# Kernel tuning notes

Hardware: AMD Instinct MI355X
Metric: run time of the kernel (lower is better)

The kernel has to match this reference:

```python
import jax, jax.numpy as jnp
import numpy as np

N_NODES, N_EDGES = 100000, 1000000
D_NODE, D_EDGE, HIDDEN = 64, 32, 64
THRESHOLD = 0.5


def _linear_params(key, out_dim, in_dim):
    # torch.nn.Linear default init: U(-1/sqrt(in), 1/sqrt(in)) for W and b
    kw, kb = jax.random.split(key)
    bound = 1.0 / np.sqrt(in_dim)
    W = jax.random.uniform(kw, (out_dim, in_dim), jnp.float32, -bound, bound)
    b = jax.random.uniform(kb, (out_dim,), jnp.float32, -bound, bound)
    return W, b


def setup_inputs() -> dict:
    key = jax.random.key(0)
    ks = jax.random.split(key, 6)
    node_features = jax.random.normal(ks[0], (N_NODES, D_NODE), jnp.float32)
    edge_index = jax.random.randint(ks[1], (2, N_EDGES), 0, N_NODES, dtype=jnp.int64)
    edge_features = jax.random.normal(ks[2], (N_EDGES, D_EDGE), jnp.float32)
    d_in = 2 * D_NODE + D_EDGE
    W1, b1 = _linear_params(ks[3], HIDDEN, d_in)
    W2, b2 = _linear_params(ks[4], HIDDEN // 2, HIDDEN)
    W3, b3 = _linear_params(ks[5], 1, HIDDEN // 2)
    return {
        "node_features": node_features,
        "edge_index": edge_index,
        "edge_features": edge_features,
        "W1": W1, "b1": b1, "W2": W2, "b2": b2, "W3": W3, "b3": b3,
    }


def reference(node_features, edge_index, edge_features, W1, b1, W2, b2, W3, b3):
    # Gather endpoint features for every edge: [E, D_NODE] each
    src = node_features[edge_index[0]]
    tgt = node_features[edge_index[1]]
    combined = jnp.concatenate([src, tgt, edge_features], axis=1)  # [E, 2*Dn+De]
    x = jax.nn.relu(combined @ W1.T + b1)
    x = jax.nn.relu(x @ W2.T + b2)
    edge_scores = jax.nn.sigmoid((x @ W3.T + b3).squeeze(-1))  # [E]
    keep_mask = edge_scores >= THRESHOLD  # edges with score < threshold removed
    return edge_scores, keep_mask
```

## Files before the change

kernel.cpp:

```cpp
#include <hip/hip_runtime.h>
#include <math.h>

#define N_NODES 100000
#define NE 1000000
#define D_NODE 64
#define D_EDGE 32
#define HID 64
#define H2C 32
#define D_IN 160
#define NTILES (NE / 16)
#define CHUNK 8
#define EPS1 1.5e-3f
#define EPS2 1e-3f

typedef __attribute__((ext_vector_type(8))) short short8;
typedef __attribute__((ext_vector_type(4))) float f32x4;

#define WS_A1_OFF 16
#define WS_A2_OFF (WS_A1_OFF + 8192)
#define WS_AS_OFF (WS_A2_OFF + 8192)
#define WS_AT_OFF (WS_AS_OFF + 16384)
#define WS_UHI    (WS_AT_OFF + 16384)
#define TBL_BYTES (N_NODES * HID * 2)
#define WS_ULO (WS_UHI + TBL_BYTES)
#define WS_VHI (WS_ULO + TBL_BYTES)
#define WS_VLO (WS_VHI + TBL_BYTES)
#define WS_MASK (WS_VLO + TBL_BYTES)
#define WS_MASK2 (WS_MASK + 125008)
#define WS_V15_MIN (WS_MASK2 + 125008 + 131072)

__device__ __forceinline__ unsigned short bf16_rne(float x) {
    unsigned int u = __float_as_uint(x);
    u += 0x7fffu + ((u >> 16) & 1u);
    return (unsigned short)(u >> 16);
}
__device__ __forceinline__ float bf16_tof(unsigned short h) {
    return __uint_as_float(((unsigned int)h) << 16);
}
__device__ __forceinline__ float h2f(unsigned short h) {
    _Float16 x = *reinterpret_cast<const _Float16*>(&h);
    return (float)x;
}
__device__ __forceinline__ unsigned short f2h(float f) {
    _Float16 x = (_Float16)f;
    return *reinterpret_cast<const unsigned short*>(&x);
}
__device__ __forceinline__ void split8(const float* xs, short8& hi, short8& lo) {
    #pragma unroll
    for (int i = 0; i < 8; ++i) {
        unsigned short h = bf16_rne(xs[i]);
        float fh = bf16_tof(h);
        unsigned short l = bf16_rne(xs[i] - fh);
        hi[i] = (short)h;
        lo[i] = (short)l;
    }
}

__global__ void prep_pack_v15(const float* __restrict__ W1, const float* __restrict__ W2,
                              unsigned char* __restrict__ ws)
{
    const int t = blockIdx.x * blockDim.x + threadIdx.x;
    if (t == 0) { *(int*)ws = 0; }
    unsigned short* a1 = (unsigned short*)(ws + WS_A1_OFF);
    unsigned short* a2 = (unsigned short*)(ws + WS_A2_OFF);
    unsigned short* as_ = (unsigned short*)(ws + WS_AS_OFF);
    unsigned short* at_ = (unsigned short*)(ws + WS_AT_OFF);
    for (int task = t; task < 1536; task += gridDim.x * blockDim.x) {
        const int l = task & 63;
        const int l15 = l & 15, kg = l >> 4;
        const float* src;
        unsigned short* dst;
        if (task < 256) {
            const int f = task >> 6;
            src = W1 + (size_t)(f*16 + l15)*D_IN + 128 + kg*8;
            dst = a1 + ((size_t)f*64 + l)*16;
        } else if (task < 512) {
            const int f = (task - 256) >> 6;
            const int nn2 = f >> 1, kk = f & 1;
            src = W2 + (size_t)(nn2*16 + l15)*HID + kk*32 + kg*8;
            dst = a2 + ((size_t)f*64 + l)*16;
        } else if (task < 1024) {
            const int f = (task - 512) >> 6;
            const int nn = f >> 1, kk = f & 1;
            src = W1 + (size_t)(nn*16 + l15)*D_IN + kk*32 + kg*8;
            dst = as_ + ((size_t)f*64 + l)*16;
        } else {
            const int f = (task - 1024) >> 6;
            const int nn = f >> 1, kk = f & 1;
            src = W1 + (size_t)(nn*16 + l15)*D_IN + 64 + kk*32 + kg*8;
            dst = at_ + ((size_t)f*64 + l)*16;
        }
        #pragma unroll
        for (int i = 0; i < 8; ++i) {
            const float wv = src[i];
            const unsigned short h = bf16_rne(wv);
            dst[i] = h;
            dst[8+i] = bf16_rne(wv - bf16_tof(h));
        }
    }
}

__global__ __launch_bounds__(256) void prep_uv_v15(
    const float* __restrict__ nf, const float* __restrict__ b1,
    const unsigned short* __restrict__ asp, const unsigned short* __restrict__ atp,
    unsigned short* __restrict__ Uhi, unsigned short* __restrict__ Ulo,
    unsigned short* __restrict__ Vhi, unsigned short* __restrict__ Vlo)
{
    __shared__ __attribute__((aligned(16))) unsigned short tb[4][16 * 64];
    const int wave = threadIdx.x >> 6, lane = threadIdx.x & 63;
    const int l15 = lane & 15, kg = lane >> 4;
    const int mt = blockIdx.x * 4 + wave;
    if (mt >= N_NODES / 16) return;
    const int node0 = mt * 16;

    const float* np_ = nf + (size_t)(node0 + l15) * 64;
    short8 ahi[2], alo[2];
    #pragma unroll
    for (int kk = 0; kk < 2; ++kk) {
        const float4 x0 = *(const float4*)(np_ + kk*32 + kg*8);
        const float4 x1 = *(const float4*)(np_ + kk*32 + kg*8 + 4);
        float xs[8] = {x0.x,x0.y,x0.z,x0.w,x1.x,x1.y,x1.z,x1.w};
        split8(xs, ahi[kk], alo[kk]);
    }
    float b1v[4];
    #pragma unroll
    for (int nn = 0; nn < 4; ++nn) b1v[nn] = b1[nn*16 + l15];

    const f32x4 z4 = {0.f,0.f,0.f,0.f};
    f32x4 au[4], av[4];
    #pragma unroll
    for (int nn = 0; nn < 4; ++nn) { au[nn] = z4; av[nn] = z4; }
    #pragma unroll
    for (int kk = 0; kk < 2; ++kk) {
        #pragma unroll
        for (int nn = 0; nn < 4; ++nn) {
            const unsigned short* fs = asp + ((size_t)(nn*2+kk)*64 + lane)*16;
            const short8 bsh = *(const short8*)fs;
            const short8 bsl = *(const short8*)(fs + 8);
            au[nn] = __builtin_amdgcn_mfma_f32_16x16x32_bf16(ahi[kk], bsh, au[nn],0,0,0);
            au[nn] = __builtin_amdgcn_mfma_f32_16x16x32_bf16(ahi[kk], bsl, au[nn],0,0,0);
            au[nn] = __builtin_amdgcn_mfma_f32_16x16x32_bf16(alo[kk], bsh, au[nn],0,0,0);
            const unsigned short* ft = atp + ((size_t)(nn*2+kk)*64 + lane)*16;
            const short8 bth = *(const short8*)ft;
            const short8 btl = *(const short8*)(ft + 8);
            av[nn] = __builtin_amdgcn_mfma_f32_16x16x32_bf16(ahi[kk], bth, av[nn],0,0,0);
            av[nn] = __builtin_amdgcn_mfma_f32_16x16x32_bf16(ahi[kk], btl, av[nn],0,0,0);
            av[nn] = __builtin_amdgcn_mfma_f32_16x16x32_bf16(alo[kk], bth, av[nn],0,0,0);
        }
    }

    unsigned short uhr[4][4], ulr[4][4], vhr[4][4], vlr[4][4];
    #pragma unroll
    for (int nn = 0; nn < 4; ++nn)
        #pragma unroll
        for (int r = 0; r < 4; ++r) {
            const float u = au[nn][r] + b1v[nn];
            const unsigned short uh_ = f2h(u);
            uhr[nn][r] = uh_; ulr[nn][r] = f2h(u - h2f(uh_));
            const float v = av[nn][r];
            const unsigned short vh_ = f2h(v);
            vhr[nn][r] = vh_; vlr[nn][r] = f2h(v - h2f(vh_));
        }

    const int tnode = lane >> 2, tsl = lane & 3;
    unsigned short* const dsts[4] = {Uhi, Ulo, Vhi, Vlo};
    #pragma unroll
    for (int pass = 0; pass < 4; ++pass) {
        #pragma unroll
        for (int nn = 0; nn < 4; ++nn)
            #pragma unroll
            for (int r = 0; r < 4; ++r)
                tb[wave][(kg*4 + r)*64 + nn*16 + l15] =
                    (pass == 0) ? uhr[nn][r] :
                    (pass == 1) ? ulr[nn][r] :
                    (pass == 2) ? vhr[nn][r] : vlr[nn][r];
        asm volatile("s_waitcnt lgkmcnt(0)" ::: "memory");
        const uint4 q0 = *(const uint4*)&tb[wave][tnode*64 + tsl*16];
        const uint4 q1 = *(const uint4*)&tb[wave][tnode*64 + tsl*16 + 8];
        unsigned short* gd = dsts[pass] + (size_t)(node0 + tnode)*64 + tsl*16;
        *(uint4*)gd = q0;
        *(uint4*)(gd + 8) = q1;
        asm volatile("s_waitcnt lgkmcnt(0)" ::: "memory");
    }
}

__global__ __launch_bounds__(256) void edge_mlp_v8_kernel(
    const int* __restrict__ ei, const float* __restrict__ ef,
    const float* __restrict__ b2, const float* __restrict__ W3, const float* __restrict__ b3,
    const unsigned short* __restrict__ a1p, const unsigned short* __restrict__ a2p,
    const unsigned short* __restrict__ Uhi, const unsigned short* __restrict__ Vhi,
    unsigned short* __restrict__ maskbuf,
    float* __restrict__ out)
{
    __shared__ __attribute__((aligned(16))) float Hs[4][16][68];
    const int wave = threadIdx.x >> 6, lane = threadIdx.x & 63;
    const int l15 = lane & 15, kg = lane >> 4;
    const long long e0 = (long long)blockIdx.x * 128 + wave * 32;

    const int is64 = (ei[1]==0)&(ei[3]==0)&(ei[5]==0)&(ei[7]==0);

    int si[2], ti[2];
    const float* efpp[2];
    #pragma unroll
    for (int t = 0; t < 2; ++t) {
        long long e = e0 + t * 16 + l15;
        if (e >= NE) e = NE - 1;
        if (is64) { si[t] = ei[(size_t)(2*e)]; ti[t] = ei[(size_t)(2*(NE+e))]; }
        else      { si[t] = ei[(size_t)e];     ti[t] = ei[(size_t)(NE+e)]; }
        efpp[t] = ef + (size_t)e * D_EDGE;
    }
    float4 efv[2][2];
    #pragma unroll
    for (int t = 0; t < 2; ++t) {
        efv[t][0] = *(const float4*)(efpp[t] + kg*8);
        efv[t][1] = *(const float4*)(efpp[t] + kg*8 + 4);
    }
    short8 uh[2][2], vh[2][2];
    #pragma unroll
    for (int t = 0; t < 2; ++t)
        #pragma unroll
        for (int kk = 0; kk < 2; ++kk) {
            uh[t][kk] = *(const short8*)(Uhi + (size_t)si[t]*64 + kk*32 + kg*8);
            vh[t][kk] = *(const short8*)(Vhi + (size_t)ti[t]*64 + kk*32 + kg*8);
        }

    const f32x4 z4 = {0.f,0.f,0.f,0.f};
    f32x4 acc1[2][4];
    #pragma unroll
    for (int t = 0; t < 2; ++t) {
        float xsl[8] = {efv[t][0].x,efv[t][0].y,efv[t][0].z,efv[t][0].w,
                        efv[t][1].x,efv[t][1].y,efv[t][1].z,efv[t][1].w};
        short8 ahi, alo;
        split8(xsl, ahi, alo);
        #pragma unroll
        for (int nn = 0; nn < 4; ++nn) {
            const unsigned short* fp = a1p + ((size_t)nn*64 + lane)*16;
            const short8 bhi = *(const short8*)fp;
            const short8 blo = *(const short8*)(fp + 8);
            f32x4 a = z4;
            a = __builtin_amdgcn_mfma_f32_16x16x32_bf16(ahi, bhi, a, 0,0,0);
            a = __builtin_amdgcn_mfma_f32_16x16x32_bf16(ahi, blo, a, 0,0,0);
            a = __builtin_amdgcn_mfma_f32_16x16x32_bf16(alo, bhi, a, 0,0,0);
            acc1[t][nn] = a;
        }
    }

    const float b2a = b2[l15], b2b = b2[16 + l15];
    const float w3a = W3[l15], w3b = W3[16 + l15];
    const float b3s = b3[0];

    #pragma unroll
    for (int t = 0; t < 2; ++t) {
        #pragma unroll
        for (int nn = 0; nn < 4; ++nn)
            #pragma unroll
            for (int r = 0; r < 4; ++r)
                Hs[wave][kg*4 + r][nn*16 + l15] = acc1[t][nn][r];
        asm volatile("s_waitcnt lgkmcnt(0)" ::: "memory");

        f32x4 acc2[2] = {z4, z4};
        #pragma unroll
        for (int kk = 0; kk < 2; ++kk) {
            const float* hp = &Hs[wave][l15][kk*32 + kg*8];
            float xsl[8];
            #pragma unroll
            for (int i = 0; i < 8; ++i)
                xsl[i] = fmaxf(hp[i] + h2f((unsigned short)uh[t][kk][i])
                                     + h2f((unsigned short)vh[t][kk][i]), 0.f);
            short8 a2hi, a2lo;
            split8(xsl, a2hi, a2lo);
            #pragma unroll
            for (int nn = 0; nn < 2; ++nn) {
                const unsigned short* fp = a2p + ((size_t)(nn*2+kk)*64 + lane)*16;
                const short8 bhi = *(const short8*)fp;
                const short8 blo = *(const short8*)(fp + 8);
                acc2[nn] = __builtin_amdgcn_mfma_f32_16x16x32_bf16(a2hi, bhi, acc2[nn],0,0,0);
                acc2[nn] = __builtin_amdgcn_mfma_f32_16x16x32_bf16(a2hi, blo, acc2[nn],0,0,0);
                acc2[nn] = __builtin_amdgcn_mfma_f32_16x16x32_bf16(a2lo, bhi, acc2[nn],0,0,0);
            }
        }
        asm volatile("s_waitcnt lgkmcnt(0)" ::: "memory");

        float vv[4];
        #pragma unroll
        for (int r = 0; r < 4; ++r) {
            float x = fmaxf(acc2[0][r] + b2a, 0.f) * w3a + fmaxf(acc2[1][r] + b2b, 0.f) * w3b;
            #pragma unroll
            for (int off = 1; off < 16; off <<= 1) x += __shfl_xor(x, off, 16);
            vv[r] = x + b3s;
        }
        float lg = 0.f;
        bool valid = false;
        long long e = 0;
        if (l15 < 4) {
            lg = (l15 == 0) ? vv[0] : (l15 == 1) ? vv[1] : (l15 == 2) ? vv[2] : vv[3];
            e = e0 + t * 16 + kg * 4 + l15;
            valid = (e < NE);
            if (valid) {
                const float sc = 1.0f / (1.0f + expf(-lg));
                out[e] = sc;
                out[NE + e] = (sc >= 0.5f) ? 1.0f : 0.0f;
            }
        }
        const bool flag = valid && (fabsf(lg) < EPS1);
        const unsigned long long m = __ballot(flag);
        const unsigned int mask16 = (unsigned int)( (m & 0xFull)
                                                  | ((m >> 12) & 0xF0ull)
                                                  | ((m >> 24) & 0xF00ull)
                                                  | ((m >> 36) & 0xF000ull) );
        const long long tile = (e0 + t * 16) >> 4;
        if (lane == 0 && tile < NTILES) maskbuf[tile] = (unsigned short)mask16;
    }
}

__global__ __launch_bounds__(256) void fixup_v16(
    const float* __restrict__ nf, const int* __restrict__ ei,
    const float* __restrict__ ef,
    const float* __restrict__ W1, const float* __restrict__ b1,
    const float* __restrict__ W2, const float* __restrict__ b2,
    const float* __restrict__ W3, const float* __restrict__ b3,
    const unsigned short* __restrict__ Uhi, const unsigned short* __restrict__ Ulo,
    const unsigned short* __restrict__ Vhi, const unsigned short* __restrict__ Vlo,
    const unsigned short* __restrict__ mask1,
    float* __restrict__ out)
{
    __shared__ float W1e[64][33];
    __shared__ float W2s[32][65];
    __shared__ float fh[4][HID];
    __shared__ double dfh[4][HID];
    __shared__ __attribute__((aligned(16))) float efs[4][32];
    __shared__ __attribute__((aligned(16))) float rows[4][160];
    __shared__ unsigned int anyflag;
    const int wave = threadIdx.x >> 6, lane = threadIdx.x & 63;
    const int wid = (blockIdx.x * blockDim.x + threadIdx.x) >> 6;
    const int base_tile = wid * CHUNK;
    const bool wave_active = (base_tile < NTILES);

    uint4 mv = make_uint4(0, 0, 0, 0);
    if (wave_active)
        mv = *(const uint4*)((const unsigned char*)mask1 + (size_t)wid * 16);
    const unsigned int any = mv.x | mv.y | mv.z | mv.w;
    if (threadIdx.x == 0) anyflag = 0;
    __syncthreads();
    if (lane == 0 && any) atomicOr(&anyflag, 1u);
    __syncthreads();
    if (anyflag == 0) return;

    for (int i = threadIdx.x; i < 64*32; i += blockDim.x)
        W1e[i >> 5][i & 31] = W1[(size_t)(i >> 5)*D_IN + 128 + (i & 31)];
    for (int i = threadIdx.x; i < 32*64; i += blockDim.x)
        W2s[i >> 6][i & 63] = W2[i];
    __syncthreads();

    const float b2l = (lane < H2C) ? b2[lane] : 0.f;
    const float w3l = (lane < H2C) ? W3[lane] : 0.f;
    const float b3s = b3[0];
    const int is64 = (ei[1]==0)&(ei[3]==0)&(ei[5]==0)&(ei[7]==0);

    if (!wave_active) return;
    const unsigned int mw[4] = {mv.x, mv.y, mv.z, mv.w};

    #pragma unroll 1
    for (int j = 0; j < CHUNK; ++j) {
        const int tile = base_tile + j;
        if (tile >= NTILES) break;
        unsigned int mask = (mw[j >> 1] >> ((j & 1) * 16)) & 0xFFFFu;
        while (mask) {
            const int b = __ffs(mask) - 1;
            mask &= mask - 1;
            const int e = tile * 16 + b;
            int si, ti;
            if (is64) { si = ei[(size_t)2*e]; ti = ei[(size_t)2*(NE + (long long)e)]; }
            else      { si = ei[e];           ti = ei[NE + (size_t)e]; }
            const float u = h2f(Uhi[(size_t)si*64 + lane]) + h2f(Ulo[(size_t)si*64 + lane]);
            const float v = h2f(Vhi[(size_t)ti*64 + lane]) + h2f(Vlo[(size_t)ti*64 + lane]);
            if (lane < 8)
                ((float4*)efs[wave])[lane] =
                    ((const float4*)(ef + (size_t)e * D_EDGE))[lane];
            asm volatile("s_waitcnt lgkmcnt(0)" ::: "memory");
            float p0 = u + v, p1 = 0.f, p2 = 0.f, p3 = 0.f;
            #pragma unroll
            for (int k = 0; k < 32; k += 4) {
                p0 = fmaf(efs[wave][k+0], W1e[lane][k+0], p0);
                p1 = fmaf(efs[wave][k+1], W1e[lane][k+1], p1);
                p2 = fmaf(efs[wave][k+2], W1e[lane][k+2], p2);
                p3 = fmaf(efs[wave][k+3], W1e[lane][k+3], p3);
            }
            fh[wave][lane] = fmaxf((p0 + p1) + (p2 + p3), 0.f);
            asm volatile("s_waitcnt lgkmcnt(0)" ::: "memory");

            float tsum = 0.f;
            if (lane < H2C) {
                float h0 = b2l, h1 = 0.f, h2 = 0.f, h3 = 0.f;
                #pragma unroll
                for (int jj = 0; jj < 64; jj += 4) {
                    h0 = fmaf(fh[wave][jj+0], W2s[lane][jj+0], h0);
                    h1 = fmaf(fh[wave][jj+1], W2s[lane][jj+1], h1);
                    h2 = fmaf(fh[wave][jj+2], W2s[lane][jj+2], h2);
                    h3 = fmaf(fh[wave][jj+3], W2s[lane][jj+3], h3);
                }
                tsum = fmaxf((h0 + h1) + (h2 + h3), 0.f) * w3l;
            }
            #pragma unroll
            for (int off = 1; off < 32; off <<= 1) tsum += __shfl_xor(tsum, off, 32);
            int refl = 0;
            if (lane == 0) {
                const float lg = tsum + b3s;
                const float sc = 1.0f / (1.0f + expf(-lg));
                out[e] = sc;
                out[NE + (size_t)e] = (sc >= 0.5f) ? 1.0f : 0.0f;
                refl = (fabsf(lg) < EPS2) ? 1 : 0;
            }
            refl = __shfl(refl, 0, 64);
            asm volatile("s_waitcnt lgkmcnt(0)" ::: "memory");

            if (refl) {
                const float* sp = nf + (size_t)si * D_NODE;
                const float* tp = nf + (size_t)ti * D_NODE;
                const float* ep = ef + (size_t)e * D_EDGE;
                if (lane < 16)      ((float4*)&rows[wave][0])[lane]        = ((const float4*)sp)[lane];
                else if (lane < 32) ((float4*)&rows[wave][64])[lane - 16]  = ((const float4*)tp)[lane - 16];
                else if (lane < 40) ((float4*)&rows[wave][128])[lane - 32] = ((const float4*)ep)[lane - 32];
                asm volatile("s_waitcnt lgkmcnt(0)" ::: "memory");

                const float* rw = rows[wave];
                double a0 = (double)b1[lane], a1 = 0.0, a2 = 0.0, a3 = 0.0;
                const float* w1r = W1 + (size_t)lane * D_IN;
                #pragma unroll 4
                for (int k = 0; k < 160; k += 4) {
                    a0 = fma((double)rw[k+0], (double)w1r[k+0], a0);
                    a1 = fma((double)rw[k+1], (double)w1r[k+1], a1);
                    a2 = fma((double)rw[k+2], (double)w1r[k+2], a2);
                    a3 = fma((double)rw[k+3], (double)w1r[k+3], a3);
                }
                dfh[wave][lane] = fmax((a0 + a1) + (a2 + a3), 0.0);
                asm volatile("s_waitcnt lgkmcnt(0)" ::: "memory");

                double dsum = 0.0;
                if (lane < H2C) {
                    double h0 = (double)b2[lane], h1 = 0.0, h2 = 0.0, h3 = 0.0;
                    const float* w2r = W2 + (size_t)lane * HID;
                    #pragma unroll 4
                    for (int jj = 0; jj < 64; jj += 4) {
                        h0 = fma(dfh[wave][jj+0], (double)w2r[jj+0], h0);
                        h1 = fma(dfh[wave][jj+1], (double)w2r[jj+1], h1);
                        h2 = fma(dfh[wave][jj+2], (double)w2r[jj+2], h2);
                        h3 = fma(dfh[wave][jj+3], (double)w2r[jj+3], h3);
                    }
                    dsum = fmax((h0 + h1) + (h2 + h3), 0.0) * (double)W3[lane];
                }
                #pragma unroll
                for (int off = 1; off < 32; off <<= 1) dsum += __shfl_xor(dsum, off, 32);
                if (lane == 0) {
                    const double logit = dsum + (double)b3[0];
                    const float sc = (float)(1.0 / (1.0 + exp(-logit)));
                    out[e] = sc;
                    out[NE + (size_t)e] = (sc >= 0.5f) ? 1.0f : 0.0f;
                }
                asm volatile("s_waitcnt lgkmcnt(0)" ::: "memory");
            }
        }
    }
}

__global__ void zero_counter_kernel(int* __restrict__ c) {
    if (blockIdx.x == 0 && threadIdx.x == 0) c[0] = 0;
}

__global__ __launch_bounds__(256, 4) void edge_mlp_f32_kernel(
    const float* __restrict__ nf, const int* __restrict__ ei,
    const float* __restrict__ ef,
    const float* __restrict__ W1, const float* __restrict__ b1,
    const float* __restrict__ W2, const float* __restrict__ b2,
    const float* __restrict__ W3, const float* __restrict__ b3,
    int* __restrict__ counter, int* __restrict__ list, int cap,
    float* __restrict__ out)
{
    const int e = blockIdx.x * blockDim.x + threadIdx.x;
    if (e >= NE) return;
    const int is64 = (ei[1]==0)&(ei[3]==0)&(ei[5]==0)&(ei[7]==0);
    int si, ti;
    if (is64) { si = ei[2*(size_t)e]; ti = ei[2*((size_t)NE + e)]; }
    else      { si = ei[e];           ti = ei[NE + e]; }
    const float* srcp = nf + (size_t)si * D_NODE;
    const float* tgtp = nf + (size_t)ti * D_NODE;
    const float* efp  = ef + (size_t)e  * D_EDGE;

    float acc[HID];
    #pragma unroll
    for (int j = 0; j < HID; ++j) acc[j] = b1[j];
    #pragma unroll 1
    for (int kc = 0; kc < D_IN / 16; ++kc) {
        const float* base = (kc < 4) ? (srcp + kc * 16)
                          : (kc < 8) ? (tgtp + (kc - 4) * 16)
                                     : (efp  + (kc - 8) * 16);
        float c[16];
        #pragma unroll
        for (int q = 0; q < 4; ++q) {
            const float4 v = *reinterpret_cast<const float4*>(base + q * 4);
            c[q*4+0]=v.x; c[q*4+1]=v.y; c[q*4+2]=v.z; c[q*4+3]=v.w;
        }
        #pragma unroll
        for (int j = 0; j < HID; ++j)
            #pragma unroll
            for (int q = 0; q < 16; ++q)
                acc[j] = fmaf(c[q], W1[j*D_IN + kc*16 + q], acc[j]);
    }
    #pragma unroll
    for (int j = 0; j < HID; ++j) acc[j] = fmaxf(acc[j], 0.0f);

    float logit = b3[0];
    #pragma unroll 1
    for (int jj = 0; jj < H2C; ++jj) {
        float h = b2[jj];
        #pragma unroll
        for (int j = 0; j < HID; ++j) h = fmaf(acc[j], W2[jj*HID + j], h);
        logit = fmaf(fmaxf(h, 0.0f), W3[jj], logit);
    }
    const float score = 1.0f / (1.0f + expf(-logit));
    out[e] = score;
    out[(size_t)NE + e] = (score >= 0.5f) ? 1.0f : 0.0f;
    if (fabsf(logit) < EPS2) {
        const int idx = atomicAdd(counter, 1);
        if (idx < cap) list[idx] = e;
    }
}

__global__ __launch_bounds__(256) void fixup_list_f64_kernel(
    const float* __restrict__ nf, const int* __restrict__ ei,
    const float* __restrict__ ef,
    const float* __restrict__ W1, const float* __restrict__ b1,
    const float* __restrict__ W2, const float* __restrict__ b2,
    const float* __restrict__ W3, const float* __restrict__ b3,
    const int* __restrict__ counter, const int* __restrict__ list, int cap,
    float* __restrict__ out)
{
    __shared__ double fh[4][HID];
    __shared__ __attribute__((aligned(16))) float rows[4][160];
    const int wave = threadIdx.x >> 6, lane = threadIdx.x & 63;
    const int nwaves = (gridDim.x * blockDim.x) >> 6;
    const int wid = (blockIdx.x * blockDim.x + threadIdx.x) >> 6;
    int n = counter[0]; if (n > cap) n = cap;
    const int is64 = (ei[1]==0)&(ei[3]==0)&(ei[5]==0)&(ei[7]==0);

    for (int i = wid; i < n; i += nwaves) {
        const int e = list[i];
        int si, ti;
        if (is64) { si = ei[(size_t)2*e]; ti = ei[(size_t)2*(NE + (long long)e)]; }
        else      { si = ei[e];           ti = ei[NE + (size_t)e]; }
        const float* sp = nf + (size_t)si * D_NODE;
        const float* tp = nf + (size_t)ti * D_NODE;
        const float* ep = ef + (size_t)e * D_EDGE;

        if (lane < 16)      ((float4*)&rows[wave][0])[lane]        = ((const float4*)sp)[lane];
        else if (lane < 32) ((float4*)&rows[wave][64])[lane - 16]  = ((const float4*)tp)[lane - 16];
        else if (lane < 40) ((float4*)&rows[wave][128])[lane - 32] = ((const float4*)ep)[lane - 32];
        asm volatile("s_waitcnt lgkmcnt(0)" ::: "memory");

        const float* rw = rows[wave];
        double a0 = (double)b1[lane], a1 = 0.0, a2 = 0.0, a3 = 0.0;
        const float* w1r = W1 + (size_t)lane * D_IN;
        #pragma unroll 4
        for (int k = 0; k < 160; k += 4) {
            a0 = fma((double)rw[k+0], (double)w1r[k+0], a0);
            a1 = fma((double)rw[k+1], (double)w1r[k+1], a1);
            a2 = fma((double)rw[k+2], (double)w1r[k+2], a2);
            a3 = fma((double)rw[k+3], (double)w1r[k+3], a3);
        }
        fh[wave][lane] = fmax((a0 + a1) + (a2 + a3), 0.0);
        asm volatile("s_waitcnt lgkmcnt(0)" ::: "memory");

        double tsum = 0.0;
        if (lane < H2C) {
            double h0 = (double)b2[lane], h1 = 0.0, h2 = 0.0, h3 = 0.0;
            const float* w2r = W2 + (size_t)lane * HID;
            #pragma unroll 4
            for (int jj = 0; jj < 64; jj += 4) {
                h0 = fma(fh[wave][jj+0], (double)w2r[jj+0], h0);
                h1 = fma(fh[wave][jj+1], (double)w2r[jj+1], h1);
                h2 = fma(fh[wave][jj+2], (double)w2r[jj+2], h2);
                h3 = fma(fh[wave][jj+3], (double)w2r[jj+3], h3);
            }
            tsum = fmax((h0 + h1) + (h2 + h3), 0.0) * (double)W3[lane];
        }
        #pragma unroll
        for (int off = 1; off < 32; off <<= 1) tsum += __shfl_xor(tsum, off, 32);
        if (lane == 0) {
            const double logit = tsum + (double)b3[0];
            const float sc = (float)(1.0 / (1.0 + exp(-logit)));
            out[e] = sc;
            out[NE + (size_t)e] = (sc >= 0.5f) ? 1.0f : 0.0f;
        }
        asm volatile("s_waitcnt lgkmcnt(0)" ::: "memory");
    }
}

extern "C" void kernel_launch(void* const* d_in, const int* in_sizes, int n_in,
                              void* d_out, int out_size, void* d_ws, size_t ws_size,
                              hipStream_t stream) {
    const float* nf = (const float*)d_in[0];
    const int*   ei = (const int*)  d_in[1];
    const float* ef = (const float*)d_in[2];
    const float* W1 = (const float*)d_in[3];
    const float* b1 = (const float*)d_in[4];
    const float* W2 = (const float*)d_in[5];
    const float* b2 = (const float*)d_in[6];
    const float* W3 = (const float*)d_in[7];
    const float* b3 = (const float*)d_in[8];
    float* out = (float*)d_out;
    unsigned char* ws = (unsigned char*)d_ws;

    if (ws_size >= (size_t)WS_V15_MIN) {
        unsigned short* Uhi = (unsigned short*)(ws + WS_UHI);
        unsigned short* Ulo = (unsigned short*)(ws + WS_ULO);
        unsigned short* Vhi = (unsigned short*)(ws + WS_VHI);
        unsigned short* Vlo = (unsigned short*)(ws + WS_VLO);
        unsigned short* mask1 = (unsigned short*)(ws + WS_MASK);
        hipLaunchKernelGGL(prep_pack_v15, dim3(6), dim3(256), 0, stream, W1, W2, ws);
        hipLaunchKernelGGL(prep_uv_v15, dim3((N_NODES/16 + 3) / 4), dim3(256), 0, stream,
                           nf, b1,
                           (const unsigned short*)(ws + WS_AS_OFF),
                           (const unsigned short*)(ws + WS_AT_OFF),
                           Uhi, Ulo, Vhi, Vlo);
        hipLaunchKernelGGL(edge_mlp_v8_kernel, dim3((NE + 127) / 128), dim3(256), 0, stream,
                           ei, ef, b2, W3, b3,
                           (const unsigned short*)(ws + WS_A1_OFF),
                           (const unsigned short*)(ws + WS_A2_OFF),
                           Uhi, Vhi, mask1, out);
        hipLaunchKernelGGL(fixup_v16, dim3(2048), dim3(256), 0, stream,
                           nf, ei, ef, W1, b1, W2, b2, W3, b3,
                           Uhi, Ulo, Vhi, Vlo, mask1, out);
    } else {
        int* counter = (int*)ws;
        long long cap_ll = ((long long)ws_size - 16) / 4;
        const int cap = (int)(cap_ll < 0 ? 0 : (cap_ll > NE ? NE : cap_ll));
        int* slist = (int*)(ws + 16);
        hipLaunchKernelGGL(zero_counter_kernel, dim3(1), dim3(64), 0, stream, counter);
        hipLaunchKernelGGL(edge_mlp_f32_kernel, dim3((NE + 255)/256), dim3(256), 0, stream,
                           nf, ei, ef, W1, b1, W2, b2, W3, b3, counter, slist, cap, out);
        hipLaunchKernelGGL(fixup_list_f64_kernel, dim3(512), dim3(256), 0, stream,
                           nf, ei, ef, W1, b1, W2, b2, W3, b3, counter, slist, cap, out);
    }
}
```

Measured before the change: 228.3 us.

## Compact flagged edges into a list before fixup for balanced work distribution

Adds a compaction kernel that scans the per-tile near-threshold masks, prefix-sums popcounts per block and appends flagged edge indices to a global list via an atomic counter. The fixup kernel then grid-strides over this compact list instead of having each wave scan a fixed chunk of tiles. This is meant to remove load imbalance and wasted blocks that scan empty masks. The cost is an extra kernel launch and list writes/reads, and the list is capped at a fixed size.

```diff
diff --git a/kernel.cpp b/kernel.cpp
--- a/kernel.cpp
+++ b/kernel.cpp
@@ -9,9 +9,10 @@
 #define H2C 32
 #define D_IN 160
 #define NTILES (NE / 16)
-#define CHUNK 8
 #define EPS1 1.5e-3f
 #define EPS2 1e-3f
+#define TILES_PER_CBLOCK 245
+#define LIST_CAP 400000
 
 typedef __attribute__((ext_vector_type(8))) short short8;
 typedef __attribute__((ext_vector_type(4))) float f32x4;
@@ -26,8 +27,8 @@
 #define WS_VHI (WS_ULO + TBL_BYTES)
 #define WS_VLO (WS_VHI + TBL_BYTES)
 #define WS_MASK (WS_VLO + TBL_BYTES)
-#define WS_MASK2 (WS_MASK + 125008)
-#define WS_V15_MIN (WS_MASK2 + 125008 + 131072)
+#define WS_LIST (WS_MASK + 125008)
+#define WS_V17_MIN (WS_LIST + LIST_CAP * 4)
 
 __device__ __forceinline__ unsigned short bf16_rne(float x) {
     unsigned int u = __float_as_uint(x);
@@ -60,7 +61,7 @@
                               unsigned char* __restrict__ ws)
 {
     const int t = blockIdx.x * blockDim.x + threadIdx.x;
-    if (t == 0) { *(int*)ws = 0; }
+    if (t == 0) { ((int*)ws)[0] = 0; ((int*)ws)[1] = 0; }
     unsigned short* a1 = (unsigned short*)(ws + WS_A1_OFF);
     unsigned short* a2 = (unsigned short*)(ws + WS_A2_OFF);
     unsigned short* as_ = (unsigned short*)(ws + WS_AS_OFF);
@@ -313,7 +314,39 @@
     }
 }
 
-__global__ __launch_bounds__(256) void fixup_v16(
+__global__ __launch_bounds__(256) void compact_v17(
+    const unsigned short* __restrict__ mask1,
+    int* __restrict__ counter, int* __restrict__ list)
+{
+    __shared__ int pref[256];
+    __shared__ int sbase;
+    const int tid = threadIdx.x;
+    const int tile = blockIdx.x * TILES_PER_CBLOCK + tid;
+    unsigned int m = 0;
+    if (tid < TILES_PER_CBLOCK && tile < NTILES) m = mask1[tile];
+    const int p = __popc(m);
+    pref[tid] = p;
+    __syncthreads();
+    #pragma unroll
+    for (int off = 1; off < 256; off <<= 1) {
+        const int v = (tid >= off) ? pref[tid - off] : 0;
+        __syncthreads();
+        pref[tid] += v;
+        __syncthreads();
+    }
+    if (tid == 255) sbase = atomicAdd(counter, pref[255]);
+    __syncthreads();
+    int pos = sbase + pref[tid] - p;
+    unsigned int mm = m;
+    while (mm) {
+        const int b = __ffs(mm) - 1;
+        mm &= mm - 1;
+        if (pos < LIST_CAP) list[pos] = tile * 16 + b;
+        ++pos;
+    }
+}
+
+__global__ __launch_bounds__(256) void fixup_list_v17(
     const float* __restrict__ nf, const int* __restrict__ ei,
     const float* __restrict__ ef,
     const float* __restrict__ W1, const float* __restrict__ b1,
@@ -321,7 +354,7 @@
     const float* __restrict__ W3, const float* __restrict__ b3,
     const unsigned short* __restrict__ Uhi, const unsigned short* __restrict__ Ulo,
     const unsigned short* __restrict__ Vhi, const unsigned short* __restrict__ Vlo,
-    const unsigned short* __restrict__ mask1,
+    const int* __restrict__ counter, const int* __restrict__ list,
     float* __restrict__ out)
 {
     __shared__ float W1e[64][33];
@@ -330,21 +363,9 @@
     __shared__ double dfh[4][HID];
     __shared__ __attribute__((aligned(16))) float efs[4][32];
     __shared__ __attribute__((aligned(16))) float rows[4][160];
-    __shared__ unsigned int anyflag;
     const int wave = threadIdx.x >> 6, lane = threadIdx.x & 63;
-    const int wid = (blockIdx.x * blockDim.x + threadIdx.x) >> 6;
-    const int base_tile = wid * CHUNK;
-    const bool wave_active = (base_tile < NTILES);
-
-    uint4 mv = make_uint4(0, 0, 0, 0);
-    if (wave_active)
-        mv = *(const uint4*)((const unsigned char*)mask1 + (size_t)wid * 16);
-    const unsigned int any = mv.x | mv.y | mv.z | mv.w;
-    if (threadIdx.x == 0) anyflag = 0;
-    __syncthreads();
-    if (lane == 0 && any) atomicOr(&anyflag, 1u);
-    __syncthreads();
-    if (anyflag == 0) return;
+    int n = counter[0]; if (n > LIST_CAP) n = LIST_CAP;
+    if (n == 0) return;
 
     for (int i = threadIdx.x; i < 64*32; i += blockDim.x)
         W1e[i >> 5][i & 31] = W1[(size_t)(i >> 5)*D_IN + 128 + (i & 31)];
@@ -356,109 +377,100 @@
     const float w3l = (lane < H2C) ? W3[lane] : 0.f;
     const float b3s = b3[0];
     const int is64 = (ei[1]==0)&(ei[3]==0)&(ei[5]==0)&(ei[7]==0);
-
-    if (!wave_active) return;
-    const unsigned int mw[4] = {mv.x, mv.y, mv.z, mv.w};
-
-    #pragma unroll 1
-    for (int j = 0; j < CHUNK; ++j) {
-        const int tile = base_tile + j;
-        if (tile >= NTILES) break;
-        unsigned int mask = (mw[j >> 1] >> ((j & 1) * 16)) & 0xFFFFu;
-        while (mask) {
-            const int b = __ffs(mask) - 1;
-            mask &= mask - 1;
-            const int e = tile * 16 + b;
-            int si, ti;
-            if (is64) { si = ei[(size_t)2*e]; ti = ei[(size_t)2*(NE + (long long)e)]; }
-            else      { si = ei[e];           ti = ei[NE + (size_t)e]; }
-            const float u = h2f(Uhi[(size_t)si*64 + lane]) + h2f(Ulo[(size_t)si*64 + lane]);
-            const float v = h2f(Vhi[(size_t)ti*64 + lane]) + h2f(Vlo[(size_t)ti*64 + lane]);
-            if (lane < 8)
-                ((float4*)efs[wave])[lane] =
-                    ((const float4*)(ef + (size_t)e * D_EDGE))[lane];
+    const int nwaves = (gridDim.x * blockDim.x) >> 6;
+    const int wid = (blockIdx.x * blockDim.x + threadIdx.x) >> 6;
+
+    for (int i = wid; i < n; i += nwaves) {
+        const int e = list[i];
+        int si, ti;
+        if (is64) { si = ei[(size_t)2*e]; ti = ei[(size_t)2*(NE + (long long)e)]; }
+        else      { si = ei[e];           ti = ei[NE + (size_t)e]; }
+        const float u = h2f(Uhi[(size_t)si*64 + lane]) + h2f(Ulo[(size_t)si*64 + lane]);
+        const float v = h2f(Vhi[(size_t)ti*64 + lane]) + h2f(Vlo[(size_t)ti*64 + lane]);
+        if (lane < 8)
+            ((float4*)efs[wave])[lane] =
+                ((const float4*)(ef + (size_t)e * D_EDGE))[lane];
+        asm volatile("s_waitcnt lgkmcnt(0)" ::: "memory");
+        float p0 = u + v, p1 = 0.f, p2 = 0.f, p3 = 0.f;
+        #pragma unroll
+        for (int k = 0; k < 32; k += 4) {
+            p0 = fmaf(efs[wave][k+0], W1e[lane][k+0], p0);
+            p1 = fmaf(efs[wave][k+1], W1e[lane][k+1], p1);
+            p2 = fmaf(efs[wave][k+2], W1e[lane][k+2], p2);
+            p3 = fmaf(efs[wave][k+3], W1e[lane][k+3], p3);
+        }
+        fh[wave][lane] = fmaxf((p0 + p1) + (p2 + p3), 0.f);
+        asm volatile("s_waitcnt lgkmcnt(0)" ::: "memory");
+
+        float tsum = 0.f;
+        if (lane < H2C) {
+            float h0 = b2l, h1 = 0.f, h2 = 0.f, h3 = 0.f;
+            #pragma unroll
+            for (int jj = 0; jj < 64; jj += 4) {
+                h0 = fmaf(fh[wave][jj+0], W2s[lane][jj+0], h0);
+                h1 = fmaf(fh[wave][jj+1], W2s[lane][jj+1], h1);
+                h2 = fmaf(fh[wave][jj+2], W2s[lane][jj+2], h2);
+                h3 = fmaf(fh[wave][jj+3], W2s[lane][jj+3], h3);
+            }
+            tsum = fmaxf((h0 + h1) + (h2 + h3), 0.f) * w3l;
+        }
+        #pragma unroll
+        for (int off = 1; off < 32; off <<= 1) tsum += __shfl_xor(tsum, off, 32);
+        int refl = 0;
+        if (lane == 0) {
+            const float lg = tsum + b3s;
+            const float sc = 1.0f / (1.0f + expf(-lg));
+            out[e] = sc;
+            out[NE + (size_t)e] = (sc >= 0.5f) ? 1.0f : 0.0f;
+            refl = (fabsf(lg) < EPS2) ? 1 : 0;
+        }
+        refl = __shfl(refl, 0, 64);
+        asm volatile("s_waitcnt lgkmcnt(0)" ::: "memory");
+
+        if (refl) {
+            const float* sp = nf + (size_t)si * D_NODE;
+            const float* tp = nf + (size_t)ti * D_NODE;
+            const float* ep = ef + (size_t)e * D_EDGE;
+            if (lane < 16)      ((float4*)&rows[wave][0])[lane]        = ((const float4*)sp)[lane];
+            else if (lane < 32) ((float4*)&rows[wave][64])[lane - 16]  = ((const float4*)tp)[lane - 16];
+            else if (lane < 40) ((float4*)&rows[wave][128])[lane - 32] = ((const float4*)ep)[lane - 32];
             asm volatile("s_waitcnt lgkmcnt(0)" ::: "memory");
-            float p0 = u + v, p1 = 0.f, p2 = 0.f, p3 = 0.f;
-            #pragma unroll
-            for (int k = 0; k < 32; k += 4) {
-                p0 = fmaf(efs[wave][k+0], W1e[lane][k+0], p0);
-                p1 = fmaf(efs[wave][k+1], W1e[lane][k+1], p1);
-                p2 = fmaf(efs[wave][k+2], W1e[lane][k+2], p2);
-                p3 = fmaf(efs[wave][k+3], W1e[lane][k+3], p3);
+
+            const float* rw = rows[wave];
+            double a0 = (double)b1[lane], a1 = 0.0, a2 = 0.0, a3 = 0.0;
+            const float* w1r = W1 + (size_t)lane * D_IN;
+            #pragma unroll 4
+            for (int k = 0; k < 160; k += 4) {
+                a0 = fma((double)rw[k+0], (double)w1r[k+0], a0);
+                a1 = fma((double)rw[k+1], (double)w1r[k+1], a1);
+                a2 = fma((double)rw[k+2], (double)w1r[k+2], a2);
+                a3 = fma((double)rw[k+3], (double)w1r[k+3], a3);
             }
-            fh[wave][lane] = fmaxf((p0 + p1) + (p2 + p3), 0.f);
+            dfh[wave][lane] = fmax((a0 + a1) + (a2 + a3), 0.0);
             asm volatile("s_waitcnt lgkmcnt(0)" ::: "memory");
 
-            float tsum = 0.f;
+            double dsum = 0.0;
             if (lane < H2C) {
-                float h0 = b2l, h1 = 0.f, h2 = 0.f, h3 = 0.f;
-                #pragma unroll
+                double h0 = (double)b2[lane], h1 = 0.0, h2 = 0.0, h3 = 0.0;
+                const float* w2r = W2 + (size_t)lane * HID;
+                #pragma unroll 4
                 for (int jj = 0; jj < 64; jj += 4) {
-                    h0 = fmaf(fh[wave][jj+0], W2s[lane][jj+0], h0);
-                    h1 = fmaf(fh[wave][jj+1], W2s[lane][jj+1], h1);
-                    h2 = fmaf(fh[wave][jj+2], W2s[lane][jj+2], h2);
-                    h3 = fmaf(fh[wave][jj+3], W2s[lane][jj+3], h3);
+                    h0 = fma(dfh[wave][jj+0], (double)w2r[jj+0], h0);
+                    h1 = fma(dfh[wave][jj+1], (double)w2r[jj+1], h1);
+                    h2 = fma(dfh[wave][jj+2], (double)w2r[jj+2], h2);
+                    h3 = fma(dfh[wave][jj+3], (double)w2r[jj+3], h3);
                 }
-                tsum = fmaxf((h0 + h1) + (h2 + h3), 0.f) * w3l;
+                dsum = fmax((h0 + h1) + (h2 + h3), 0.0) * (double)W3[lane];
             }
             #pragma unroll
-            for (int off = 1; off < 32; off <<= 1) tsum += __shfl_xor(tsum, off, 32);
-            int refl = 0;
+            for (int off = 1; off < 32; off <<= 1) dsum += __shfl_xor(dsum, off, 32);
             if (lane == 0) {
-                const float lg = tsum + b3s;
-                const float sc = 1.0f / (1.0f + expf(-lg));
+                const double logit = dsum + (double)b3[0];
+                const float sc = (float)(1.0 / (1.0 + exp(-logit)));
                 out[e] = sc;
                 out[NE + (size_t)e] = (sc >= 0.5f) ? 1.0f : 0.0f;
-                refl = (fabsf(lg) < EPS2) ? 1 : 0;
             }
-            refl = __shfl(refl, 0, 64);
             asm volatile("s_waitcnt lgkmcnt(0)" ::: "memory");
-
-            if (refl) {
-                const float* sp = nf + (size_t)si * D_NODE;
-                const float* tp = nf + (size_t)ti * D_NODE;
-                const float* ep = ef + (size_t)e * D_EDGE;
-                if (lane < 16)      ((float4*)&rows[wave][0])[lane]        = ((const float4*)sp)[lane];
-                else if (lane < 32) ((float4*)&rows[wave][64])[lane - 16]  = ((const float4*)tp)[lane - 16];
-                else if (lane < 40) ((float4*)&rows[wave][128])[lane - 32] = ((const float4*)ep)[lane - 32];
-                asm volatile("s_waitcnt lgkmcnt(0)" ::: "memory");
-
-                const float* rw = rows[wave];
-                double a0 = (double)b1[lane], a1 = 0.0, a2 = 0.0, a3 = 0.0;
-                const float* w1r = W1 + (size_t)lane * D_IN;
-                #pragma unroll 4
-                for (int k = 0; k < 160; k += 4) {
-                    a0 = fma((double)rw[k+0], (double)w1r[k+0], a0);
-                    a1 = fma((double)rw[k+1], (double)w1r[k+1], a1);
-                    a2 = fma((double)rw[k+2], (double)w1r[k+2], a2);
-                    a3 = fma((double)rw[k+3], (double)w1r[k+3], a3);
-                }
-                dfh[wave][lane] = fmax((a0 + a1) + (a2 + a3), 0.0);
-                asm volatile("s_waitcnt lgkmcnt(0)" ::: "memory");
-
-                double dsum = 0.0;
-                if (lane < H2C) {
-                    double h0 = (double)b2[lane], h1 = 0.0, h2 = 0.0, h3 = 0.0;
-                    const float* w2r = W2 + (size_t)lane * HID;
-                    #pragma unroll 4
-                    for (int jj = 0; jj < 64; jj += 4) {
-                        h0 = fma(dfh[wave][jj+0], (double)w2r[jj+0], h0);
-                        h1 = fma(dfh[wave][jj+1], (double)w2r[jj+1], h1);
-                        h2 = fma(dfh[wave][jj+2], (double)w2r[jj+2], h2);
-                        h3 = fma(dfh[wave][jj+3], (double)w2r[jj+3], h3);
-                    }
-                    dsum = fmax((h0 + h1) + (h2 + h3), 0.0) * (double)W3[lane];
-                }
-                #pragma unroll
-                for (int off = 1; off < 32; off <<= 1) dsum += __shfl_xor(dsum, off, 32);
-                if (lane == 0) {
-                    const double logit = dsum + (double)b3[0];
-                    const float sc = (float)(1.0 / (1.0 + exp(-logit)));
-                    out[e] = sc;
-                    out[NE + (size_t)e] = (sc >= 0.5f) ? 1.0f : 0.0f;
-                }
-                asm volatile("s_waitcnt lgkmcnt(0)" ::: "memory");
-            }
         }
     }
 }
@@ -610,12 +622,14 @@
     float* out = (float*)d_out;
     unsigned char* ws = (unsigned char*)d_ws;
 
-    if (ws_size >= (size_t)WS_V15_MIN) {
+    if (ws_size >= (size_t)WS_V17_MIN) {
         unsigned short* Uhi = (unsigned short*)(ws + WS_UHI);
         unsigned short* Ulo = (unsigned short*)(ws + WS_ULO);
         unsigned short* Vhi = (unsigned short*)(ws + WS_VHI);
         unsigned short* Vlo = (unsigned short*)(ws + WS_VLO);
         unsigned short* mask1 = (unsigned short*)(ws + WS_MASK);
+        int* counter = (int*)ws;
+        int* list = (int*)(ws + WS_LIST);
         hipLaunchKernelGGL(prep_pack_v15, dim3(6), dim3(256), 0, stream, W1, W2, ws);
         hipLaunchKernelGGL(prep_uv_v15, dim3((N_NODES/16 + 3) / 4), dim3(256), 0, stream,
                            nf, b1,
@@ -627,9 +641,11 @@
                            (const unsigned short*)(ws + WS_A1_OFF),
                            (const unsigned short*)(ws + WS_A2_OFF),
                            Uhi, Vhi, mask1, out);
-        hipLaunchKernelGGL(fixup_v16, dim3(2048), dim3(256), 0, stream,
+        hipLaunchKernelGGL(compact_v17, dim3(256), dim3(256), 0, stream,
+                           mask1, counter, list);
+        hipLaunchKernelGGL(fixup_list_v17, dim3(2048), dim3(256), 0, stream,
                            nf, ei, ef, W1, b1, W2, b2, W3, b3,
-                           Uhi, Ulo, Vhi, Vlo, mask1, out);
+                           Uhi, Ulo, Vhi, Vlo, counter, list, out);
     } else {
         int* counter = (int*)ws;
         long long cap_ll = ((long long)ws_size - 16) / 4;
```

Result: faster. 213.1 us, median of 2 (-6.7%).
